# Kernel tuning notes

Hardware: AMD Instinct MI355X
Metric: run time of the kernel (lower is better)

The kernel has to match this reference:

```python
import jax, jax.numpy as jnp
import numpy as np

N_NODES = 20000
DEG = 32
N_EDGES = N_NODES * DEG
NUM_USERS = 100000
D = 128


def setup_inputs() -> dict:
    key = jax.random.key(0)
    ks = jax.random.split(key, 10)
    nodes = jax.random.randint(ks[0], (N_NODES,), 0, NUM_USERS)
    neigh_idx = jax.random.randint(ks[1], (N_EDGES,), 0, NUM_USERS)
    # fixed-degree flattening of the ragged to_neighs lists: every node has DEG neighbors
    seg_ids = jnp.repeat(jnp.arange(N_NODES), DEG)
    u2e = jax.random.normal(ks[2], (NUM_USERS, D), dtype=jnp.float32)
    W1 = jax.random.normal(ks[3], (2 * D, D), dtype=jnp.float32) * 0.05
    b1 = jax.random.normal(ks[4], (D,), dtype=jnp.float32) * 0.05
    W2 = jax.random.normal(ks[5], (D, D), dtype=jnp.float32) * 0.05
    b2 = jax.random.normal(ks[6], (D,), dtype=jnp.float32) * 0.05
    w3 = jax.random.normal(ks[7], (D, 1), dtype=jnp.float32) * 0.05
    b3 = jax.random.normal(ks[8], (1,), dtype=jnp.float32) * 0.05
    return {"nodes": nodes, "neigh_idx": neigh_idx, "seg_ids": seg_ids,
            "u2e": u2e, "W1": W1, "b1": b1, "W2": W2, "b2": b2, "w3": w3, "b3": b3}


def reference(nodes, neigh_idx, seg_ids, u2e, W1, b1, W2, b2, w3, b3):
    n = nodes.shape[0]
    e_u = u2e[neigh_idx]                 # [E, D] neighbor embeddings
    u_rep = u2e[nodes][seg_ids]          # [E, D] center-node embedding repeated per neighbor
    x = jnp.concatenate([e_u, u_rep], axis=1)        # [E, 2D]
    h = jax.nn.relu(x @ W1 + b1)                      # [E, D]
    h = jax.nn.relu(h @ W2 + b2)                      # [E, D]
    s = (h @ w3 + b3)[:, 0]                           # [E] attention logits
    # segment softmax over each node's neighbor set
    smax = jax.ops.segment_max(s, seg_ids, num_segments=n)
    e = jnp.exp(s - smax[seg_ids])
    denom = jax.ops.segment_sum(e, seg_ids, num_segments=n)
    att = e / denom[seg_ids]                          # [E]
    # attention-weighted neighbor sum (e_u^T @ att per node)
    out = jax.ops.segment_sum(att[:, None] * e_u, seg_ids, num_segments=n)  # [N, D]
    return out
```

## Files before the change

kernel.cpp:

```cpp
#include <hip/hip_runtime.h>
#include <hip/hip_bf16.h>

#define DD 128
#define DEG 32

typedef __attribute__((ext_vector_type(8))) _Float16 half8;
typedef __attribute__((ext_vector_type(4))) float f32x4;

__device__ __forceinline__ unsigned pkh(float a, float b) {
    _Float16 ha = (_Float16)a, hb = (_Float16)b;
    return (unsigned)__builtin_bit_cast(unsigned short, ha)
         | ((unsigned)__builtin_bit_cast(unsigned short, hb) << 16);
}
__device__ __forceinline__ float h2f_lo(unsigned u) {
    return (float)__builtin_bit_cast(_Float16, (unsigned short)(u & 0xffff));
}
__device__ __forceinline__ float h2f_hi(unsigned u) {
    return (float)__builtin_bit_cast(_Float16, (unsigned short)(u >> 16));
}

__global__ __launch_bounds__(256) void k_aux(
    const float* __restrict__ W1, const float* __restrict__ W2,
    const float4* __restrict__ u2e4, uint4* __restrict__ w1img,
    uint4* __restrict__ w2t, uint4* __restrict__ ub16v, int total8)
{
    const int bid = blockIdx.x;
    if (bid < 24) {
        int t = bid * 256 + threadIdx.x;
        if (t < 4096) {
            int l = t & 63, f = t >> 6, k4 = f & 3, nt = f >> 2;
            int n = nt * 16 + (l & 15), kb = k4 * 32 + ((l >> 4) & 3) * 8;
            float v[8];
            #pragma unroll
            for (int i = 0; i < 8; ++i) {
                int k = kb + i;
                v[i] = (n < DD) ? W1[k * DD + n] : W1[(DD + k) * DD + (n - DD)];
            }
            uint4 r;
            r.x = pkh(v[0], v[1]); r.y = pkh(v[2], v[3]);
            r.z = pkh(v[4], v[5]); r.w = pkh(v[6], v[7]);
            w1img[t] = r;
        } else if (t < 6144) {
            int q = t - 4096;
            int l = q & 63, f = q >> 6, k4 = f & 3, mt = f >> 2;
            int ch = mt * 16 + (l & 15), kb = k4 * 32 + ((l >> 4) & 3) * 8;
            float v[8];
            #pragma unroll
            for (int i = 0; i < 8; ++i) v[i] = W2[(kb + i) * DD + ch];
            uint4 r;
            r.x = pkh(v[0], v[1]); r.y = pkh(v[2], v[3]);
            r.z = pkh(v[4], v[5]); r.w = pkh(v[6], v[7]);
            w2t[q] = r;
        }
    } else {
        int i = (bid - 24) * 256 + threadIdx.x;
        if (i < total8) {
            float4 v0 = u2e4[(size_t)i * 2], v1 = u2e4[(size_t)i * 2 + 1];
            uint4 r;
            r.x = pkh(v0.x, v0.y); r.y = pkh(v0.z, v0.w);
            r.z = pkh(v1.x, v1.y); r.w = pkh(v1.z, v1.w);
            ub16v[i] = r;
        }
    }
}

__global__ __launch_bounds__(256) void k_qn(
    const int* __restrict__ nodes, const float* __restrict__ u2e,
    const uint4* __restrict__ w1img, const float* __restrict__ b1,
    unsigned short* __restrict__ Qnh, int n)
{
    const int t = threadIdx.x, w = t >> 6, l = t & 63;
    const int base = blockIdx.x * 128;

    half8 a[2][4];
    #pragma unroll
    for (int nt = 0; nt < 2; ++nt) {
        int row = min(base + w * 32 + nt * 16 + (l & 15), n - 1);
        int user = nodes[row];
        const float* rp = u2e + (size_t)user * DD + ((l >> 4) << 3);
        #pragma unroll
        for (int k4 = 0; k4 < 4; ++k4) {
            float4 v0 = *reinterpret_cast<const float4*>(rp + k4 * 32);
            float4 v1 = *reinterpret_cast<const float4*>(rp + k4 * 32 + 4);
            uint4 r;
            r.x = pkh(v0.x, v0.y); r.y = pkh(v0.z, v0.w);
            r.z = pkh(v1.x, v1.y); r.w = pkh(v1.z, v1.w);
            a[nt][k4] = __builtin_bit_cast(half8, r);
        }
    }
    const int chq = (l >> 4) << 2;
    #pragma unroll
    for (int mt = 0; mt < 8; ++mt) {
        half8 wf[4];
        #pragma unroll
        for (int k4 = 0; k4 < 4; ++k4)
            wf[k4] = __builtin_bit_cast(half8, w1img[((8 + mt) * 4 + k4) * 64 + l]);
        float4 b1v = *reinterpret_cast<const float4*>(&b1[mt * 16 + chq]);
        #pragma unroll
        for (int nt = 0; nt < 2; ++nt) {
            f32x4 acc = {0.f, 0.f, 0.f, 0.f};
            #pragma unroll
            for (int k4 = 0; k4 < 4; ++k4)
                acc = __builtin_amdgcn_mfma_f32_16x16x32_f16(wf[k4], a[nt][k4], acc, 0, 0, 0);
            int row = base + w * 32 + nt * 16 + (l & 15);
            if (row < n) {
                uint2 pk;
                pk.x = pkh(acc[0] + b1v.x, acc[1] + b1v.y);
                pk.y = pkh(acc[2] + b1v.z, acc[3] + b1v.w);
                *reinterpret_cast<uint2*>(&Qnh[(size_t)row * DD + mt * 16 + chq]) = pk;
            }
        }
    }
}

__global__ __launch_bounds__(256, 4) void k_node(
    const int* __restrict__ neigh, const _Float16* __restrict__ ub16,
    const unsigned short* __restrict__ Qnh, const uint4* __restrict__ w1img,
    const uint4* __restrict__ w2t, const float* __restrict__ b2,
    const float* __restrict__ w3, float4* __restrict__ out4, int n)
{
    const int t = threadIdx.x, w = t >> 6, l = t & 63;
    const int node = min(blockIdx.x * 4 + w, n - 1);
    const int g = l >> 4, c = l & 15;

    const int idx0 = neigh[node * DEG + c];
    const int idx1 = neigh[node * DEG + 16 + c];
    const int koff = g * 8;
    half8 ub0[4], ub1[4];
    #pragma unroll
    for (int k4 = 0; k4 < 4; ++k4)
        ub0[k4] = *reinterpret_cast<const half8*>(&ub16[(size_t)idx0 * DD + k4 * 32 + koff]);
    #pragma unroll
    for (int k4 = 0; k4 < 4; ++k4)
        ub1[k4] = *reinterpret_cast<const half8*>(&ub16[(size_t)idx1 * DD + k4 * 32 + koff]);
    uint2 qnh[8];
    #pragma unroll
    for (int mt = 0; mt < 8; ++mt)
        qnh[mt] = *reinterpret_cast<const uint2*>(&Qnh[(size_t)node * DD + mt * 16 + g * 4]);

    const int srcA = ((g & 1) << 5) + c;
    const int hiSel = g >> 1;
    half8 hb0[4], hb1[4];
    #pragma unroll
    for (int k4 = 0; k4 < 4; ++k4) {
        uint2 hpA0, hpA1, hpB0, hpB1;
        {
            const int mt = 2 * k4;
            half8 wf[4];
            #pragma unroll
            for (int kk = 0; kk < 4; ++kk)
                wf[kk] = __builtin_bit_cast(half8, w1img[(mt * 4 + kk) * 64 + l]);
            f32x4 a0 = {0.f, 0.f, 0.f, 0.f}, a1 = {0.f, 0.f, 0.f, 0.f};
            #pragma unroll
            for (int kk = 0; kk < 4; ++kk)
                a0 = __builtin_amdgcn_mfma_f32_16x16x32_f16(wf[kk], ub0[kk], a0, 0, 0, 0);
            #pragma unroll
            for (int kk = 0; kk < 4; ++kk)
                a1 = __builtin_amdgcn_mfma_f32_16x16x32_f16(wf[kk], ub1[kk], a1, 0, 0, 0);
            float q0 = h2f_lo(qnh[mt].x), q1 = h2f_hi(qnh[mt].x);
            float q2 = h2f_lo(qnh[mt].y), q3 = h2f_hi(qnh[mt].y);
            hpA0.x = pkh(fmaxf(a0[0] + q0, 0.f), fmaxf(a0[1] + q1, 0.f));
            hpA0.y = pkh(fmaxf(a0[2] + q2, 0.f), fmaxf(a0[3] + q3, 0.f));
            hpB0.x = pkh(fmaxf(a1[0] + q0, 0.f), fmaxf(a1[1] + q1, 0.f));
            hpB0.y = pkh(fmaxf(a1[2] + q2, 0.f), fmaxf(a1[3] + q3, 0.f));
        }
        {
            const int mt = 2 * k4 + 1;
            half8 wf[4];
            #pragma unroll
            for (int kk = 0; kk < 4; ++kk)
                wf[kk] = __builtin_bit_cast(half8, w1img[(mt * 4 + kk) * 64 + l]);
            f32x4 a0 = {0.f, 0.f, 0.f, 0.f}, a1 = {0.f, 0.f, 0.f, 0.f};
            #pragma unroll
            for (int kk = 0; kk < 4; ++kk)
                a0 = __builtin_amdgcn_mfma_f32_16x16x32_f16(wf[kk], ub0[kk], a0, 0, 0, 0);
            #pragma unroll
            for (int kk = 0; kk < 4; ++kk)
                a1 = __builtin_amdgcn_mfma_f32_16x16x32_f16(wf[kk], ub1[kk], a1, 0, 0, 0);
            float q0 = h2f_lo(qnh[mt].x), q1 = h2f_hi(qnh[mt].x);
            float q2 = h2f_lo(qnh[mt].y), q3 = h2f_hi(qnh[mt].y);
            hpA1.x = pkh(fmaxf(a0[0] + q0, 0.f), fmaxf(a0[1] + q1, 0.f));
            hpA1.y = pkh(fmaxf(a0[2] + q2, 0.f), fmaxf(a0[3] + q3, 0.f));
            hpB1.x = pkh(fmaxf(a1[0] + q0, 0.f), fmaxf(a1[1] + q1, 0.f));
            hpB1.y = pkh(fmaxf(a1[2] + q2, 0.f), fmaxf(a1[3] + q3, 0.f));
        }
        unsigned d[4], e[4];
        #pragma unroll
        for (int j = 0; j < 4; ++j) {
            int src = srcA + ((j >> 1) << 4);
            unsigned vE = (unsigned)__shfl((int)((j & 1) ? hpA0.y : hpA0.x), src);
            unsigned vO = (unsigned)__shfl((int)((j & 1) ? hpA1.y : hpA1.x), src);
            d[j] = hiSel ? vO : vE;
            unsigned uE = (unsigned)__shfl((int)((j & 1) ? hpB0.y : hpB0.x), src);
            unsigned uO = (unsigned)__shfl((int)((j & 1) ? hpB1.y : hpB1.x), src);
            e[j] = hiSel ? uO : uE;
        }
        uint4 du = {d[0], d[1], d[2], d[3]};
        uint4 eu = {e[0], e[1], e[2], e[3]};
        hb0[k4] = __builtin_bit_cast(half8, du);
        hb1[k4] = __builtin_bit_cast(half8, eu);
    }

    float pl0 = 0.f, pl1 = 0.f;
    #pragma unroll
    for (int mt = 0; mt < 8; ++mt) {
        half8 wf[4];
        #pragma unroll
        for (int k4 = 0; k4 < 4; ++k4)
            wf[k4] = __builtin_bit_cast(half8, w2t[(mt * 4 + k4) * 64 + l]);
        float4 b2v = *reinterpret_cast<const float4*>(&b2[mt * 16 + g * 4]);
        float4 w3v = *reinterpret_cast<const float4*>(&w3[mt * 16 + g * 4]);
        f32x4 a0 = {0.f, 0.f, 0.f, 0.f}, a1 = {0.f, 0.f, 0.f, 0.f};
        #pragma unroll
        for (int k4 = 0; k4 < 4; ++k4)
            a0 = __builtin_amdgcn_mfma_f32_16x16x32_f16(wf[k4], hb0[k4], a0, 0, 0, 0);
        #pragma unroll
        for (int k4 = 0; k4 < 4; ++k4)
            a1 = __builtin_amdgcn_mfma_f32_16x16x32_f16(wf[k4], hb1[k4], a1, 0, 0, 0);
        pl0 += fmaxf(a0[0] + b2v.x, 0.f) * w3v.x + fmaxf(a0[1] + b2v.y, 0.f) * w3v.y
             + fmaxf(a0[2] + b2v.z, 0.f) * w3v.z + fmaxf(a0[3] + b2v.w, 0.f) * w3v.w;
        pl1 += fmaxf(a1[0] + b2v.x, 0.f) * w3v.x + fmaxf(a1[1] + b2v.y, 0.f) * w3v.y
             + fmaxf(a1[2] + b2v.z, 0.f) * w3v.z + fmaxf(a1[3] + b2v.w, 0.f) * w3v.w;
    }
    pl0 += __shfl_xor(pl0, 16); pl0 += __shfl_xor(pl0, 32);
    pl1 += __shfl_xor(pl1, 16); pl1 += __shfl_xor(pl1, 32);

    float mx = fmaxf(pl0, pl1);
    #pragma unroll
    for (int mask = 1; mask <= 8; mask <<= 1) mx = fmaxf(mx, __shfl_xor(mx, mask));
    float e0 = __expf(pl0 - mx), e1 = __expf(pl1 - mx);
    float sm = e0 + e1;
    #pragma unroll
    for (int mask = 1; mask <= 8; mask <<= 1) sm += __shfl_xor(sm, mask);
    float inv = __frcp_rn(sm);
    float att0 = e0 * inv, att1 = e1 * inv;

    float o[4][8];
    #pragma unroll
    for (int k4 = 0; k4 < 4; ++k4)
        #pragma unroll
        for (int i = 0; i < 8; ++i)
            o[k4][i] = att0 * (float)ub0[k4][i] + att1 * (float)ub1[k4][i];
    #pragma unroll
    for (int mask = 1; mask <= 8; mask <<= 1) {
        #pragma unroll
        for (int k4 = 0; k4 < 4; ++k4)
            #pragma unroll
            for (int i = 0; i < 8; ++i)
                o[k4][i] += __shfl_xor(o[k4][i], mask);
    }
    if (c == 0) {
        #pragma unroll
        for (int k4 = 0; k4 < 4; ++k4) {
            float4 r0 = make_float4(o[k4][0], o[k4][1], o[k4][2], o[k4][3]);
            float4 r1 = make_float4(o[k4][4], o[k4][5], o[k4][6], o[k4][7]);
            out4[(size_t)node * 32 + k4 * 8 + g * 2]     = r0;
            out4[(size_t)node * 32 + k4 * 8 + g * 2 + 1] = r1;
        }
    }
}

extern "C" void kernel_launch(void* const* d_in, const int* in_sizes, int n_in,
                              void* d_out, int out_size, void* d_ws, size_t ws_size,
                              hipStream_t stream)
{
    const int*   nodes = (const int*)  d_in[0];
    const int*   neigh = (const int*)  d_in[1];
    const float* u2e   = (const float*)d_in[3];
    const float* W1    = (const float*)d_in[4];
    const float* b1    = (const float*)d_in[5];
    const float* W2    = (const float*)d_in[6];
    const float* b2    = (const float*)d_in[7];
    const float* w3    = (const float*)d_in[8];

    const int n = in_sizes[0];
    const int U = in_sizes[3] / DD;

    uint4*          w1img = (uint4*)d_ws;
    uint4*          w2t   = w1img + 4096;
    _Float16*       ub16  = (_Float16*)(w2t + 2048);
    unsigned short* Qnh   = (unsigned short*)(ub16 + (size_t)U * DD);

    const int total8 = U * (DD / 8);

    k_aux<<<24 + (total8 + 255) / 256, 256, 0, stream>>>(
        W1, W2, (const float4*)u2e, w1img, w2t, (uint4*)ub16, total8);
    k_qn<<<(n + 127) / 128, 256, 0, stream>>>(nodes, u2e, w1img, b1, Qnh, n);
    k_node<<<(n + 3) / 4, 256, 0, stream>>>(neigh, ub16, Qnh, w1img, w2t,
                                            b2, w3, (float4*)d_out, n);
}
```

Measured before the change: 111.8 us.

## Stage weights in LDS and loop five nodes per wave with gather prefetch

```diff
diff --git a/kernel.cpp b/kernel.cpp
--- a/kernel.cpp
+++ b/kernel.cpp
@@ -113,149 +113,185 @@
     }
 }
 
-__global__ __launch_bounds__(256, 4) void k_node(
+__global__ __launch_bounds__(512, 4) void k_node(
     const int* __restrict__ neigh, const _Float16* __restrict__ ub16,
     const unsigned short* __restrict__ Qnh, const uint4* __restrict__ w1img,
     const uint4* __restrict__ w2t, const float* __restrict__ b2,
     const float* __restrict__ w3, float4* __restrict__ out4, int n)
 {
+    __shared__ uint4 s_img[4096];
+
     const int t = threadIdx.x, w = t >> 6, l = t & 63;
-    const int node = min(blockIdx.x * 4 + w, n - 1);
     const int g = l >> 4, c = l & 15;
-
-    const int idx0 = neigh[node * DEG + c];
-    const int idx1 = neigh[node * DEG + 16 + c];
     const int koff = g * 8;
-    half8 ub0[4], ub1[4];
-    #pragma unroll
-    for (int k4 = 0; k4 < 4; ++k4)
-        ub0[k4] = *reinterpret_cast<const half8*>(&ub16[(size_t)idx0 * DD + k4 * 32 + koff]);
-    #pragma unroll
-    for (int k4 = 0; k4 < 4; ++k4)
-        ub1[k4] = *reinterpret_cast<const half8*>(&ub16[(size_t)idx1 * DD + k4 * 32 + koff]);
-    uint2 qnh[8];
-    #pragma unroll
-    for (int mt = 0; mt < 8; ++mt)
-        qnh[mt] = *reinterpret_cast<const uint2*>(&Qnh[(size_t)node * DD + mt * 16 + g * 4]);
+    const int base = blockIdx.x * 40 + w * 5;
+
+    half8 ub0[2][4], ub1[2][4];
+    {
+        int node0 = min(base, n - 1);
+        int i0 = neigh[node0 * DEG + c];
+        int i1 = neigh[node0 * DEG + 16 + c];
+        #pragma unroll
+        for (int k4 = 0; k4 < 4; ++k4)
+            ub0[0][k4] = *reinterpret_cast<const half8*>(
+                &ub16[(size_t)i0 * DD + k4 * 32 + koff]);
+        #pragma unroll
+        for (int k4 = 0; k4 < 4; ++k4)
+            ub1[0][k4] = *reinterpret_cast<const half8*>(
+                &ub16[(size_t)i1 * DD + k4 * 32 + koff]);
+    }
+
+    #pragma unroll
+    for (int i = 0; i < 4; ++i) s_img[i * 512 + t] = w1img[i * 512 + t];
+    #pragma unroll
+    for (int i = 0; i < 4; ++i) s_img[2048 + i * 512 + t] = w2t[i * 512 + t];
+    __syncthreads();
 
     const int srcA = ((g & 1) << 5) + c;
     const int hiSel = g >> 1;
-    half8 hb0[4], hb1[4];
-    #pragma unroll
-    for (int k4 = 0; k4 < 4; ++k4) {
-        uint2 hpA0, hpA1, hpB0, hpB1;
-        {
-            const int mt = 2 * k4;
+
+    #pragma unroll
+    for (int it = 0; it < 5; ++it) {
+        const int cur = it & 1, nxt = cur ^ 1;
+        const int node = min(base + it, n - 1);
+
+        uint2 qnh[8];
+        #pragma unroll
+        for (int mt = 0; mt < 8; ++mt)
+            qnh[mt] = *reinterpret_cast<const uint2*>(
+                &Qnh[(size_t)node * DD + mt * 16 + g * 4]);
+
+        half8 hb0[4], hb1[4];
+        #pragma unroll
+        for (int k4 = 0; k4 < 4; ++k4) {
+            uint2 hpA0, hpA1, hpB0, hpB1;
+            {
+                const int mt = 2 * k4;
+                half8 wf[4];
+                #pragma unroll
+                for (int kk = 0; kk < 4; ++kk)
+                    wf[kk] = __builtin_bit_cast(half8, s_img[(mt * 4 + kk) * 64 + l]);
+                f32x4 a0 = {0.f, 0.f, 0.f, 0.f}, a1 = {0.f, 0.f, 0.f, 0.f};
+                #pragma unroll
+                for (int kk = 0; kk < 4; ++kk)
+                    a0 = __builtin_amdgcn_mfma_f32_16x16x32_f16(wf[kk], ub0[cur][kk], a0, 0, 0, 0);
+                #pragma unroll
+                for (int kk = 0; kk < 4; ++kk)
+                    a1 = __builtin_amdgcn_mfma_f32_16x16x32_f16(wf[kk], ub1[cur][kk], a1, 0, 0, 0);
+                float q0 = h2f_lo(qnh[mt].x), q1 = h2f_hi(qnh[mt].x);
+                float q2 = h2f_lo(qnh[mt].y), q3 = h2f_hi(qnh[mt].y);
+                hpA0.x = pkh(fmaxf(a0[0] + q0, 0.f), fmaxf(a0[1] + q1, 0.f));
+                hpA0.y = pkh(fmaxf(a0[2] + q2, 0.f), fmaxf(a0[3] + q3, 0.f));
+                hpB0.x = pkh(fmaxf(a1[0] + q0, 0.f), fmaxf(a1[1] + q1, 0.f));
+                hpB0.y = pkh(fmaxf(a1[2] + q2, 0.f), fmaxf(a1[3] + q3, 0.f));
+            }
+            {
+                const int mt = 2 * k4 + 1;
+                half8 wf[4];
+                #pragma unroll
+                for (int kk = 0; kk < 4; ++kk)
+                    wf[kk] = __builtin_bit_cast(half8, s_img[(mt * 4 + kk) * 64 + l]);
+                f32x4 a0 = {0.f, 0.f, 0.f, 0.f}, a1 = {0.f, 0.f, 0.f, 0.f};
+                #pragma unroll
+                for (int kk = 0; kk < 4; ++kk)
+                    a0 = __builtin_amdgcn_mfma_f32_16x16x32_f16(wf[kk], ub0[cur][kk], a0, 0, 0, 0);
+                #pragma unroll
+                for (int kk = 0; kk < 4; ++kk)
+                    a1 = __builtin_amdgcn_mfma_f32_16x16x32_f16(wf[kk], ub1[cur][kk], a1, 0, 0, 0);
+                float q0 = h2f_lo(qnh[mt].x), q1 = h2f_hi(qnh[mt].x);
+                float q2 = h2f_lo(qnh[mt].y), q3 = h2f_hi(qnh[mt].y);
+                hpA1.x = pkh(fmaxf(a0[0] + q0, 0.f), fmaxf(a0[1] + q1, 0.f));
+                hpA1.y = pkh(fmaxf(a0[2] + q2, 0.f), fmaxf(a0[3] + q3, 0.f));
+                hpB1.x = pkh(fmaxf(a1[0] + q0, 0.f), fmaxf(a1[1] + q1, 0.f));
+                hpB1.y = pkh(fmaxf(a1[2] + q2, 0.f), fmaxf(a1[3] + q3, 0.f));
+            }
+            unsigned d[4], e[4];
+            #pragma unroll
+            for (int j = 0; j < 4; ++j) {
+                int src = srcA + ((j >> 1) << 4);
+                unsigned vE = (unsigned)__shfl((int)((j & 1) ? hpA0.y : hpA0.x), src);
+                unsigned vO = (unsigned)__shfl((int)((j & 1) ? hpA1.y : hpA1.x), src);
+                d[j] = hiSel ? vO : vE;
+                unsigned uE = (unsigned)__shfl((int)((j & 1) ? hpB0.y : hpB0.x), src);
+                unsigned uO = (unsigned)__shfl((int)((j & 1) ? hpB1.y : hpB1.x), src);
+                e[j] = hiSel ? uO : uE;
+            }
+            uint4 du = {d[0], d[1], d[2], d[3]};
+            uint4 eu = {e[0], e[1], e[2], e[3]};
+            hb0[k4] = __builtin_bit_cast(half8, du);
+            hb1[k4] = __builtin_bit_cast(half8, eu);
+        }
+
+        if (it < 4) {
+            int nn = min(base + it + 1, n - 1);
+            int j0 = neigh[nn * DEG + c];
+            int j1 = neigh[nn * DEG + 16 + c];
+            #pragma unroll
+            for (int k4 = 0; k4 < 4; ++k4)
+                ub0[nxt][k4] = *reinterpret_cast<const half8*>(
+                    &ub16[(size_t)j0 * DD + k4 * 32 + koff]);
+            #pragma unroll
+            for (int k4 = 0; k4 < 4; ++k4)
+                ub1[nxt][k4] = *reinterpret_cast<const half8*>(
+                    &ub16[(size_t)j1 * DD + k4 * 32 + koff]);
+        }
+
+        float pl0 = 0.f, pl1 = 0.f;
+        #pragma unroll
+        for (int mt = 0; mt < 8; ++mt) {
             half8 wf[4];
             #pragma unroll
-            for (int kk = 0; kk < 4; ++kk)
-                wf[kk] = __builtin_bit_cast(half8, w1img[(mt * 4 + kk) * 64 + l]);
+            for (int k4 = 0; k4 < 4; ++k4)
+                wf[k4] = __builtin_bit_cast(half8, s_img[2048 + (mt * 4 + k4) * 64 + l]);
+            float4 b2v = *reinterpret_cast<const float4*>(&b2[mt * 16 + g * 4]);
+            float4 w3v = *reinterpret_cast<const float4*>(&w3[mt * 16 + g * 4]);
             f32x4 a0 = {0.f, 0.f, 0.f, 0.f}, a1 = {0.f, 0.f, 0.f, 0.f};
             #pragma unroll
-            for (int kk = 0; kk < 4; ++kk)
-                a0 = __builtin_amdgcn_mfma_f32_16x16x32_f16(wf[kk], ub0[kk], a0, 0, 0, 0);
-            #pragma unroll
-            for (int kk = 0; kk < 4; ++kk)
-                a1 = __builtin_amdgcn_mfma_f32_16x16x32_f16(wf[kk], ub1[kk], a1, 0, 0, 0);
-            float q0 = h2f_lo(qnh[mt].x), q1 = h2f_hi(qnh[mt].x);
-            float q2 = h2f_lo(qnh[mt].y), q3 = h2f_hi(qnh[mt].y);
-            hpA0.x = pkh(fmaxf(a0[0] + q0, 0.f), fmaxf(a0[1] + q1, 0.f));
-            hpA0.y = pkh(fmaxf(a0[2] + q2, 0.f), fmaxf(a0[3] + q3, 0.f));
-            hpB0.x = pkh(fmaxf(a1[0] + q0, 0.f), fmaxf(a1[1] + q1, 0.f));
-            hpB0.y = pkh(fmaxf(a1[2] + q2, 0.f), fmaxf(a1[3] + q3, 0.f));
-        }
-        {
-            const int mt = 2 * k4 + 1;
-            half8 wf[4];
-            #pragma unroll
-            for (int kk = 0; kk < 4; ++kk)
-                wf[kk] = __builtin_bit_cast(half8, w1img[(mt * 4 + kk) * 64 + l]);
-            f32x4 a0 = {0.f, 0.f, 0.f, 0.f}, a1 = {0.f, 0.f, 0.f, 0.f};
-            #pragma unroll
-            for (int kk = 0; kk < 4; ++kk)
-                a0 = __builtin_amdgcn_mfma_f32_16x16x32_f16(wf[kk], ub0[kk], a0, 0, 0, 0);
-            #pragma unroll
-            for (int kk = 0; kk < 4; ++kk)
-                a1 = __builtin_amdgcn_mfma_f32_16x16x32_f16(wf[kk], ub1[kk], a1, 0, 0, 0);
-            float q0 = h2f_lo(qnh[mt].x), q1 = h2f_hi(qnh[mt].x);
-            float q2 = h2f_lo(qnh[mt].y), q3 = h2f_hi(qnh[mt].y);
-            hpA1.x = pkh(fmaxf(a0[0] + q0, 0.f), fmaxf(a0[1] + q1, 0.f));
-            hpA1.y = pkh(fmaxf(a0[2] + q2, 0.f), fmaxf(a0[3] + q3, 0.f));
-            hpB1.x = pkh(fmaxf(a1[0] + q0, 0.f), fmaxf(a1[1] + q1, 0.f));
-            hpB1.y = pkh(fmaxf(a1[2] + q2, 0.f), fmaxf(a1[3] + q3, 0.f));
-        }
-        unsigned d[4], e[4];
-        #pragma unroll
-        for (int j = 0; j < 4; ++j) {
-            int src = srcA + ((j >> 1) << 4);
-            unsigned vE = (unsigned)__shfl((int)((j & 1) ? hpA0.y : hpA0.x), src);
-            unsigned vO = (unsigned)__shfl((int)((j & 1) ? hpA1.y : hpA1.x), src);
-            d[j] = hiSel ? vO : vE;
-            unsigned uE = (unsigned)__shfl((int)((j & 1) ? hpB0.y : hpB0.x), src);
-            unsigned uO = (unsigned)__shfl((int)((j & 1) ? hpB1.y : hpB1.x), src);
-            e[j] = hiSel ? uO : uE;
-        }
-        uint4 du = {d[0], d[1], d[2], d[3]};
-        uint4 eu = {e[0], e[1], e[2], e[3]};
-        hb0[k4] = __builtin_bit_cast(half8, du);
-        hb1[k4] = __builtin_bit_cast(half8, eu);
-    }
-
-    float pl0 = 0.f, pl1 = 0.f;
-    #pragma unroll
-    for (int mt = 0; mt < 8; ++mt) {
-        half8 wf[4];
+            for (int k4 = 0; k4 < 4; ++k4)
+                a0 = __builtin_amdgcn_mfma_f32_16x16x32_f16(wf[k4], hb0[k4], a0, 0, 0, 0);
+            #pragma unroll
+            for (int k4 = 0; k4 < 4; ++k4)
+                a1 = __builtin_amdgcn_mfma_f32_16x16x32_f16(wf[k4], hb1[k4], a1, 0, 0, 0);
+            pl0 += fmaxf(a0[0] + b2v.x, 0.f) * w3v.x + fmaxf(a0[1] + b2v.y, 0.f) * w3v.y
+                 + fmaxf(a0[2] + b2v.z, 0.f) * w3v.z + fmaxf(a0[3] + b2v.w, 0.f) * w3v.w;
+            pl1 += fmaxf(a1[0] + b2v.x, 0.f) * w3v.x + fmaxf(a1[1] + b2v.y, 0.f) * w3v.y
+                 + fmaxf(a1[2] + b2v.z, 0.f) * w3v.z + fmaxf(a1[3] + b2v.w, 0.f) * w3v.w;
+        }
+        pl0 += __shfl_xor(pl0, 16); pl0 += __shfl_xor(pl0, 32);
+        pl1 += __shfl_xor(pl1, 16); pl1 += __shfl_xor(pl1, 32);
+
+        float mx = fmaxf(pl0, pl1);
+        #pragma unroll
+        for (int mask = 1; mask <= 8; mask <<= 1) mx = fmaxf(mx, __shfl_xor(mx, mask));
+        float e0 = __expf(pl0 - mx), e1 = __expf(pl1 - mx);
+        float sm = e0 + e1;
+        #pragma unroll
+        for (int mask = 1; mask <= 8; mask <<= 1) sm += __shfl_xor(sm, mask);
+        float inv = __frcp_rn(sm);
+        float att0 = e0 * inv, att1 = e1 * inv;
+
+        float o[4][8];
         #pragma unroll
         for (int k4 = 0; k4 < 4; ++k4)
-            wf[k4] = __builtin_bit_cast(half8, w2t[(mt * 4 + k4) * 64 + l]);
-        float4 b2v = *reinterpret_cast<const float4*>(&b2[mt * 16 + g * 4]);
-        float4 w3v = *reinterpret_cast<const float4*>(&w3[mt * 16 + g * 4]);
-        f32x4 a0 = {0.f, 0.f, 0.f, 0.f}, a1 = {0.f, 0.f, 0.f, 0.f};
-        #pragma unroll
-        for (int k4 = 0; k4 < 4; ++k4)
-            a0 = __builtin_amdgcn_mfma_f32_16x16x32_f16(wf[k4], hb0[k4], a0, 0, 0, 0);
-        #pragma unroll
-        for (int k4 = 0; k4 < 4; ++k4)
-            a1 = __builtin_amdgcn_mfma_f32_16x16x32_f16(wf[k4], hb1[k4], a1, 0, 0, 0);
-        pl0 += fmaxf(a0[0] + b2v.x, 0.f) * w3v.x + fmaxf(a0[1] + b2v.y, 0.f) * w3v.y
-             + fmaxf(a0[2] + b2v.z, 0.f) * w3v.z + fmaxf(a0[3] + b2v.w, 0.f) * w3v.w;
-        pl1 += fmaxf(a1[0] + b2v.x, 0.f) * w3v.x + fmaxf(a1[1] + b2v.y, 0.f) * w3v.y
-             + fmaxf(a1[2] + b2v.z, 0.f) * w3v.z + fmaxf(a1[3] + b2v.w, 0.f) * w3v.w;
-    }
-    pl0 += __shfl_xor(pl0, 16); pl0 += __shfl_xor(pl0, 32);
-    pl1 += __shfl_xor(pl1, 16); pl1 += __shfl_xor(pl1, 32);
-
-    float mx = fmaxf(pl0, pl1);
-    #pragma unroll
-    for (int mask = 1; mask <= 8; mask <<= 1) mx = fmaxf(mx, __shfl_xor(mx, mask));
-    float e0 = __expf(pl0 - mx), e1 = __expf(pl1 - mx);
-    float sm = e0 + e1;
-    #pragma unroll
-    for (int mask = 1; mask <= 8; mask <<= 1) sm += __shfl_xor(sm, mask);
-    float inv = __frcp_rn(sm);
-    float att0 = e0 * inv, att1 = e1 * inv;
-
-    float o[4][8];
-    #pragma unroll
-    for (int k4 = 0; k4 < 4; ++k4)
-        #pragma unroll
-        for (int i = 0; i < 8; ++i)
-            o[k4][i] = att0 * (float)ub0[k4][i] + att1 * (float)ub1[k4][i];
-    #pragma unroll
-    for (int mask = 1; mask <= 8; mask <<= 1) {
-        #pragma unroll
-        for (int k4 = 0; k4 < 4; ++k4)
             #pragma unroll
             for (int i = 0; i < 8; ++i)
-                o[k4][i] += __shfl_xor(o[k4][i], mask);
-    }
-    if (c == 0) {
-        #pragma unroll
-        for (int k4 = 0; k4 < 4; ++k4) {
-            float4 r0 = make_float4(o[k4][0], o[k4][1], o[k4][2], o[k4][3]);
-            float4 r1 = make_float4(o[k4][4], o[k4][5], o[k4][6], o[k4][7]);
-            out4[(size_t)node * 32 + k4 * 8 + g * 2]     = r0;
-            out4[(size_t)node * 32 + k4 * 8 + g * 2 + 1] = r1;
+                o[k4][i] = att0 * (float)ub0[cur][k4][i] + att1 * (float)ub1[cur][k4][i];
+        #pragma unroll
+        for (int mask = 1; mask <= 8; mask <<= 1) {
+            #pragma unroll
+            for (int k4 = 0; k4 < 4; ++k4)
+                #pragma unroll
+                for (int i = 0; i < 8; ++i)
+                    o[k4][i] += __shfl_xor(o[k4][i], mask);
+        }
+        if (c == 0) {
+            #pragma unroll
+            for (int k4 = 0; k4 < 4; ++k4) {
+                float4 r0 = make_float4(o[k4][0], o[k4][1], o[k4][2], o[k4][3]);
+                float4 r1 = make_float4(o[k4][4], o[k4][5], o[k4][6], o[k4][7]);
+                out4[(size_t)node * 32 + k4 * 8 + g * 2]     = r0;
+                out4[(size_t)node * 32 + k4 * 8 + g * 2 + 1] = r1;
+            }
         }
     }
 }
@@ -286,6 +322,6 @@
     k_aux<<<24 + (total8 + 255) / 256, 256, 0, stream>>>(
         W1, W2, (const float4*)u2e, w1img, w2t, (uint4*)ub16, total8);
     k_qn<<<(n + 127) / 128, 256, 0, stream>>>(nodes, u2e, w1img, b1, Qnh, n);
-    k_node<<<(n + 3) / 4, 256, 0, stream>>>(neigh, ub16, Qnh, w1img, w2t,
-                                            b2, w3, (float4*)d_out, n);
-}
+    k_node<<<512, 512, 0, stream>>>(neigh, ub16, Qnh, w1img, w2t,
+                                    b2, w3, (float4*)d_out, n);
+}
```

After: 106.7 us. -4.6%, faster.
